# Kernel tuning notes

Measured on AMD Instinct MI355X. Metric: run time of the kernel, lower is better.

The kernel has to match this reference:

```python
import jax, jax.numpy as jnp
import numpy as np

S, M, E, K, C = 4096, 512, 16, 2, 128
H1, H2, H3 = 500, 500, 2000
SAMPLE = int(np.percentile(np.arange(S), 90))  # = 3685, matches int(np.percentile(idx_set, 90))
KMUL, KNUM = 2.0, 5


def setup_inputs() -> dict:
    key = jax.random.key(0)
    ks = jax.random.split(key, 8)
    def init(k, shape, fan):
        return (jax.random.normal(k, shape, jnp.float32) / np.float32(np.sqrt(fan)))
    inp = {
        'x': jax.random.normal(ks[0], (S, M), jnp.float32),
        'noise': jax.random.uniform(ks[1], (S, E), jnp.float32),
        'Wr': jnp.zeros((E, M), jnp.float32),  # router weight is zeroed in reset_parameters
        'W1': init(ks[2], (E, H1, M), M), 'b1': jnp.zeros((E, H1), jnp.float32),
        'W2': init(ks[3], (E, H2, H1), H1), 'b2': jnp.zeros((E, H2), jnp.float32),
        'W3': init(ks[4], (E, H3, H2), H2), 'b3': jnp.zeros((E, H3), jnp.float32),
        'W4': init(ks[5], (E, C, H3), H3), 'b4': jnp.zeros((E, C), jnp.float32),
    }
    rng = np.random.RandomState(0)
    npairs = K * (K - 1) // 2
    inp['idx1'] = jnp.asarray(np.stack([rng.choice(S, SAMPLE, replace=False) for _ in range(npairs)]).astype(np.int32))
    inp['idx2'] = jnp.asarray(np.stack([rng.choice(S, SAMPLE, replace=False) for _ in range(npairs)]).astype(np.int32))
    return inp


def _mmd(source, target):
    # Gaussian-kernel MMD, same math as MMD_loss (fix_sigma=None path).
    ns = source.shape[0]
    n = ns + target.shape[0]
    total = jnp.concatenate([source, target], axis=0)            # [n, d]
    sq = jnp.sum(total * total, axis=-1)
    d2 = sq[:, None] + sq[None, :] - 2.0 * (total @ total.T)     # [n, n] squared L2
    bw = jax.lax.stop_gradient(d2).sum() / (n * n - n)           # .data in torch => stop_gradient
    bw = bw / (KMUL ** (KNUM // 2))
    kern = jnp.zeros_like(d2)
    for i in range(KNUM):
        kern = kern + jnp.exp(-d2 / (bw * (KMUL ** i)))
    xx = kern[:ns, :ns]
    yy = kern[ns:, ns:]
    xy = kern[:ns, ns:]
    yx = kern[ns:, :ns]
    return jnp.mean(xx + yy - xy - yx)


def _forward(x, noise, Wr, W1, b1, W2, b2, W3, b3, W4, b4, idx1, idx2):
    select = x @ Wr.T + noise                                    # [S, E]
    gate, index = jax.lax.top_k(select, K)                       # [S, K]
    mask = jax.nn.one_hot(index, E, dtype=select.dtype)          # [S, K, E]
    density = mask.mean(axis=-2)                                 # [S, E]
    density_proxy = select.mean(axis=-2)                         # [E]
    balance_loss = jnp.mean(density_proxy * density) * float(E ** 2)
    mask_flat = mask.sum(axis=-1)                                # [S, K] (all ones)
    combine = jnp.transpose(gate[..., None] * mask_flat[..., None] * mask, (0, 2, 1))  # [S, E, K]
    dispatch = (combine != 0).astype(combine.dtype)              # bool().to(dtype)
    select0 = dispatch
    expert_inputs = jnp.einsum('sm,sec->ecm', x, dispatch)       # [E, K, M]
    h = jax.nn.relu(jnp.einsum('ecm,ehm->ech', expert_inputs, W1) + b1[:, None, :])
    h = jax.nn.relu(jnp.einsum('ech,egh->ecg', h, W2) + b2[:, None, :])
    h = jax.nn.relu(jnp.einsum('ecg,efg->ecf', h, W3) + b3[:, None, :])
    eout = jnp.einsum('ecf,edf->ecd', h, W4) + b4[:, None, :]    # [E, K, C]
    middle = jnp.transpose(jnp.einsum('sec,ecm->scm', combine, eout), (1, 0, 2))  # [K, S, C]
    output = jnp.einsum('sec,ecm->sm', combine, eout)            # [S, C]
    dist_loss = jnp.float32(0.0)
    p = 0
    for i in range(K):
        for j in range(i + 1, K):
            dist_loss = dist_loss - _mmd(middle[i][idx1[p]], middle[j][idx2[p]])
            p += 1
    return output, select0, balance_loss, dist_loss


def reference(x, noise, Wr, W1, b1, W2, b2, W3, b3, W4, b4, idx1, idx2):
    return _forward(x, noise, Wr, W1, b1, W2, b2, W3, b3, W4, b4, idx1, idx2)
```

## Files before the change

kernel.cpp:

```cpp
#include <hip/hip_runtime.h>

constexpr int S = 4096, M = 512, E = 16, CC = 128;
constexpr int H1 = 500, H2 = 500, H3 = 2000;
constexpr int TB = 256;

__global__ void k_route(const float* __restrict__ x, const float* __restrict__ noise,
                        const float* __restrict__ Wr, int* __restrict__ i0, int* __restrict__ i1,
                        float* __restrict__ g0, float* __restrict__ g1,
                        float* __restrict__ sel0, float* __restrict__ selpart,
                        int* __restrict__ counters) {
  if (blockIdx.x == 0 && threadIdx.x == 0) { counters[0] = 0; }
  int wid = threadIdx.x >> 6, lane = threadIdx.x & 63;
  int s = blockIdx.x * 4 + wid;
  const float* xr = x + (size_t)s * M;
  float xv[8];
#pragma unroll
  for (int c = 0; c < 8; ++c) xv[c] = xr[lane + 64 * c];
  float v[E];
#pragma unroll
  for (int e = 0; e < E; ++e) {
    const float* wr = Wr + (size_t)e * M;
    float acc = 0.f;
#pragma unroll
    for (int c = 0; c < 8; ++c) acc = fmaf(xv[c], wr[lane + 64 * c], acc);
#pragma unroll
    for (int off = 32; off; off >>= 1) acc += __shfl_xor(acc, off);
    v[e] = acc + noise[s * E + e];
  }
  int a0 = 0; float m0 = v[0];
#pragma unroll
  for (int e = 1; e < E; ++e) if (v[e] > m0) { m0 = v[e]; a0 = e; }
  int a1 = -1; float m1 = -3.4e38f;
#pragma unroll
  for (int e = 0; e < E; ++e) if (e != a0 && v[e] > m1) { m1 = v[e]; a1 = e; }
  __shared__ float vsh[4][16];
  if (lane < 16) vsh[wid][lane] = v[lane];
  if (lane == 0) { i0[s] = a0; i1[s] = a1; g0[s] = m0; g1[s] = m1; }
  if (lane < 16) {
    int e = lane;
    sel0[(size_t)s * 32 + e * 2 + 0] = (e == a0 && m0 != 0.f) ? 1.f : 0.f;
    sel0[(size_t)s * 32 + e * 2 + 1] = (e == a1 && m1 != 0.f) ? 1.f : 0.f;
  }
  __syncthreads();
  if (threadIdx.x < 16) {
    int e = threadIdx.x;
    selpart[blockIdx.x * 16 + e] = vsh[0][e] + vsh[1][e] + vsh[2][e] + vsh[3][e];
  }
}

__global__ __launch_bounds__(1024) void k_gather(const float* __restrict__ x,
                        const int* __restrict__ i0, const int* __restrict__ i1,
                        const float* __restrict__ g0, const float* __restrict__ g1,
                        float* __restrict__ ei) {
  __shared__ int rsi[S];
  __shared__ float rsg[S];
  __shared__ float gacc[8][128];
  int b = blockIdx.x;
  int chunk = b & 3, ek = b >> 2;
  int k = ek & 1, e = ek >> 1;
  const int* route = k ? i1 : i0;
  const float* gg = k ? g1 : g0;
  int t = threadIdx.x;
  for (int i = t; i < S; i += 1024) { rsi[i] = route[i]; rsg[i] = gg[i]; }
  __syncthreads();
  int g = t >> 7, dl = t & 127;
  int d = chunk * 128 + dl;
  float acc = 0.f;
  int q0 = g * 512;
  for (int q = q0; q < q0 + 512; ++q) {
    if (rsi[q] == e && rsg[q] != 0.f) acc += x[(size_t)q * M + d];
  }
  gacc[g][dl] = acc;
  __syncthreads();
  if (t < 128) {
    float ssum = 0.f;
#pragma unroll
    for (int g2 = 0; g2 < 8; ++g2) ssum += gacc[g2][t];
    ei[ek * M + chunk * 128 + t] = ssum;
  }
}

template <int DIN, int HOUT, bool RELU>
__global__ void k_layer(const float* __restrict__ in, const float* __restrict__ W,
                        const float* __restrict__ bias, float* __restrict__ out) {
  int w = (blockIdx.x * blockDim.x + threadIdx.x) >> 6;
  int lane = threadIdx.x & 63;
  if (w >= E * HOUT) return;
  int e = w / HOUT, h = w - e * HOUT;
  const float* wr = W + ((size_t)e * HOUT + h) * DIN;
  const float* in0 = in + (size_t)(e * 2 + 0) * DIN;
  const float* in1 = in + (size_t)(e * 2 + 1) * DIN;
  float a0 = 0.f, a1 = 0.f;
  for (int m = lane; m < DIN; m += 64) {
    float wv = wr[m];
    a0 += wv * in0[m];
    a1 += wv * in1[m];
  }
#pragma unroll
  for (int off = 32; off; off >>= 1) {
    a0 += __shfl_xor(a0, off);
    a1 += __shfl_xor(a1, off);
  }
  if (lane == 0) {
    float bb = bias[e * HOUT + h];
    float o0 = a0 + bb, o1 = a1 + bb;
    if (RELU) { o0 = fmaxf(o0, 0.f); o1 = fmaxf(o1, 0.f); }
    out[(size_t)(e * 2 + 0) * HOUT + h] = o0;
    out[(size_t)(e * 2 + 1) * HOUT + h] = o1;
  }
}

__global__ __launch_bounds__(256) void k_gprep(const float* __restrict__ eo,
                        const float* __restrict__ selpart,
                        const int* __restrict__ idx1, const int* __restrict__ idx2,
                        const int* __restrict__ i0, const int* __restrict__ i1,
                        const float* __restrict__ g0, const float* __restrict__ g1,
                        float* __restrict__ G32, float* __restrict__ rowg,
                        int* __restrict__ rowe, float* __restrict__ wpart,
                        int* __restrict__ cpart,
                        float* __restrict__ outb, int ns, int ncnt, int npad) {
  int t = threadIdx.x;
  if (blockIdx.x == 0) {
    __shared__ float Es[32 * 132];
    __shared__ double red_d[256];
    __shared__ float dpl[16];
    for (int i = t; i < 32 * 128; i += 256) Es[(i >> 7) * 132 + (i & 127)] = eo[i];
    __syncthreads();
    for (int p = t; p < 1024; p += 256) {
      int u = p >> 5, v = p & 31;
      float s = 0.f;
#pragma unroll 8
      for (int d = 0; d < 128; ++d) s = fmaf(Es[u * 132 + d], Es[v * 132 + d], s);
      G32[p] = s;
    }
    int e2 = t & 15, r0 = t >> 4;
    double acc = 0.0;
    for (int b2 = r0; b2 < 1024; b2 += 16) acc += (double)selpart[b2 * 16 + e2];
    red_d[t] = acc;
    __syncthreads();
    for (int off = 128; off >= 16; off >>= 1) { if (t < off) red_d[t] += red_d[t + off]; __syncthreads(); }
    if (t < 16) dpl[t] = (float)(red_d[t] / (double)S);
    __syncthreads();
    double acc2 = 0.0;
    for (int s2 = t; s2 < S; s2 += 256) acc2 += 0.5 * ((double)dpl[i0[s2]] + (double)dpl[i1[s2]]);
    red_d[t] = acc2;
    __syncthreads();
    for (int off = 128; off; off >>= 1) { if (t < off) red_d[t] += red_d[t + off]; __syncthreads(); }
    if (t == 0) outb[0] = (float)(red_d[0] / 256.0);
    return;
  }
  int blk = blockIdx.x - 1;
  int r = blk * 256 + t;
  float g = 0.f; int ek = 0;
  bool valid = (r < npad);
  if (r < ns)        { int tk = idx1[r];      ek = i0[tk] * 2 + 0; g = g0[tk]; }
  else if (r < ncnt) { int tk = idx2[r - ns]; ek = i1[tk] * 2 + 1; g = g1[tk]; }
  if (valid) { rowg[r] = g; rowe[r] = ek; }
  int ekb = valid ? ek : -1;
  __shared__ float sw[4][32], sw2[4][32];
  __shared__ int sc[4][32];
  int lane = t & 63, w = t >> 6;
  float g2 = g * g;
  for (int e = 0; e < 32; ++e) {
    unsigned long long m = __ballot(ekb == e);
    float vw = (ekb == e) ? g : 0.f;
    float vw2 = (ekb == e) ? g2 : 0.f;
#pragma unroll
    for (int off = 32; off; off >>= 1) { vw += __shfl_xor(vw, off); vw2 += __shfl_xor(vw2, off); }
    if (lane == 0) { sw[w][e] = vw; sw2[w][e] = vw2; sc[w][e] = __popcll(m); }
  }
  __syncthreads();
  if (t < 32) {
    wpart[blk * 64 + t]      = sw[0][t] + sw[1][t] + sw[2][t] + sw[3][t];
    wpart[blk * 64 + 32 + t] = sw2[0][t] + sw2[1][t] + sw2[2][t] + sw2[3][t];
    cpart[blk * 32 + t]      = sc[0][t] + sc[1][t] + sc[2][t] + sc[3][t];
  }
}

__global__ __launch_bounds__(256) void k_mid(const float* __restrict__ G32,
                        const float* __restrict__ wpart, const int* __restrict__ cpart,
                        const float* __restrict__ rowg, const int* __restrict__ rowe,
                        float* __restrict__ srowg, float* __restrict__ srowA,
                        int* __restrict__ srowe, float* __restrict__ srowsg,
                        float* __restrict__ cl2,
                        int ns, int ncnt, int npad, int nrowblk) {
  __shared__ int cpl[32 * 32];
  __shared__ int total_s[32];
  __shared__ int offmy[32];
  __shared__ float wf[32], w2f[32];
  __shared__ double redd[256];
  __shared__ int wcnt[4][32];
  __shared__ float c_sh;
  int t = threadIdx.x, blk = blockIdx.x;
  for (int i = t; i < nrowblk * 32; i += 256) cpl[i] = cpart[i];
  if (t < 32) {
    float sw = 0.f, sw2 = 0.f;
    for (int b = 0; b < nrowblk; ++b) { sw += wpart[b * 64 + t]; sw2 += wpart[b * 64 + 32 + t]; }
    wf[t] = sw; w2f[t] = sw2;
  }
  __syncthreads();
  if (t < 32) {
    int tot = 0;
    for (int b = 0; b < nrowblk; ++b) tot += cpl[b * 32 + t];
    total_s[t] = tot;
  }
  __syncthreads();
  if (t < 32) {
    int off = 0;
    for (int e = 0; e < t; ++e) off += total_s[e];
    for (int b = 0; b < blk; ++b) off += cpl[b * 32 + t];
    offmy[t] = off;
  }
  double part = 0.0;
  for (int i = t; i < 1024; i += 256)
    part += (double)wf[i >> 5] * (double)wf[i & 31] * (double)G32[i];
  redd[t] = part;
  __syncthreads();
  for (int off = 128; off; off >>= 1) { if (t < off) redd[t] += redd[t + off]; __syncthreads(); }
  double wGw = redd[0];
  __syncthreads();
  redd[t] = (t < 32) ? (double)w2f[t] * (double)G32[t * 33] : 0.0;
  __syncthreads();
  for (int off = 128; off; off >>= 1) { if (t < off) redd[t] += redd[t + off]; __syncthreads(); }
  if (t == 0) {
    double nn = (double)ncnt;
    double sumd2 = 2.0 * nn * redd[0] - 2.0 * wGw;
    double bw = sumd2 / (nn * nn - nn) / 4.0;
    c_sh = (float)(1.0 / (bw * 16.0));
    if (blk == 0) cl2[0] = c_sh;
  }
  __syncthreads();
  float c = c_sh;
  int r = blk * 256 + t;
  bool valid = (r < npad);
  float g = valid ? rowg[r] : 0.f;
  int ek = valid ? rowe[r] : -1;
  float sg = (r < ns) ? 1.f : (r < ncnt ? -1.f : 0.f);
  int lane = t & 63, w = t >> 6;
  int myrank = 0;
  for (int e = 0; e < 32; ++e) {
    unsigned long long m = __ballot(ek == e);
    if (ek == e) myrank = __popcll(m & ((1ull << lane) - 1ull));
    if (lane == 0) wcnt[w][e] = __popcll(m);
  }
  __syncthreads();
  if (valid) {
    int woff = 0;
    for (int w2 = 0; w2 < w; ++w2) woff += wcnt[w2][ek];
    int dest = offmy[ek] + woff + myrank;
    srowg[dest] = g;
    srowsg[dest] = sg;
    srowe[dest] = ek;
    srowA[dest] = c * g * g * G32[ek * 33];
  }
}

__global__ __launch_bounds__(512) void k_tail(const float* __restrict__ eo,
                      const int* __restrict__ i0, const int* __restrict__ i1,
                      const float* __restrict__ g0, const float* __restrict__ g1,
                      float* __restrict__ out,
                      const float* __restrict__ srowg, const float* __restrict__ srowA,
                      const int* __restrict__ srowe, const float* __restrict__ srowsg,
                      const float* __restrict__ G32, const float* __restrict__ cl2,
                      double* __restrict__ bsum, float* __restrict__ out_dist,
                      int ns, int ncnt, int nt, int ntri, int* __restrict__ counters) {
  int b = blockIdx.x, tid = threadIdx.x;
  if (b >= ntri) {
    int idx = (b - ntri) * 512 + tid;
    int s = idx >> 7, d = idx & (CC - 1);
    out[idx] = g0[s] * eo[(i0[s] * 2 + 0) * CC + d] + g1[s] * eo[(i1[s] * 2 + 1) * CC + d];
    return;
  }
  __shared__ float K2[1056];
  __shared__ float gAs[264], aAs[264], sAs[264];
  __shared__ int   eAs[264];
  __shared__ float gBs[264], aBs[264], sBs[264];
  __shared__ int   eBs[264];
  __shared__ float wred[8];
  __shared__ double redd[512];
  __shared__ int lastflag;

  int L = b;
  int bi = 0, rem = L;
  while (rem >= nt - bi) { rem -= nt - bi; ++bi; }
  int bj = bi + rem;
  const int ib = bi * TB, jb = bj * TB;

  float c = cl2[0];
  for (int i = tid; i < 1024; i += 512) K2[(i >> 5) * 33 + (i & 31)] = 2.f * c * G32[i];
  if (tid < TB) {
    int r = tid, p = (r & 7) * 33 + (r >> 3);
    gAs[p] = srowg[ib + r]; aAs[p] = srowA[ib + r];
    eAs[p] = srowe[ib + r] * 33; sAs[p] = srowsg[ib + r];
  } else {
    int r = tid - TB, p = (r & 7) * 33 + (r >> 3);
    gBs[p] = srowg[jb + r]; aBs[p] = srowA[jb + r];
    eBs[p] = srowe[jb + r]; sBs[p] = srowsg[jb + r];
  }
  __syncthreads();

  int ti = tid & 15, tjj = tid >> 4;
  float gj[8], Aj[8], sgj[8]; int ej[8];
#pragma unroll
  for (int q = 0; q < 8; ++q) {
    int p = q * 33 + tjj;
    gj[q] = gBs[p]; Aj[q] = aBs[p]; ej[q] = eBs[p]; sgj[q] = sBs[p];
  }
  float tsum = 0.f;
#pragma unroll
  for (int rb = 0; rb < 2; ++rb) {
    float gi[8], Ai[8], sgi[8]; int ei[8];
#pragma unroll
    for (int r = 0; r < 8; ++r) {
      int p = r * 33 + ti * 2 + rb;
      gi[r] = gAs[p]; Ai[r] = aAs[p]; ei[r] = eAs[p]; sgi[r] = sAs[p];
    }
#pragma unroll
    for (int r = 0; r < 8; ++r) {
#pragma unroll
      for (int q = 0; q < 8; ++q) {
        float gg = gi[r] * gj[q];
        float arg = fmaf(K2[ei[r] + ej[q]], gg, -(Ai[r] + Aj[q]));
        float t = __expf(arg);
        float t2 = t * t;   float s5 = t + t2;
        float t4 = t2 * t2; s5 += t4;
        float t8 = t4 * t4; s5 += t8;
        float t16 = t8 * t8; s5 += t16;
        tsum = fmaf(sgi[r] * sgj[q], s5, tsum);
      }
    }
  }
#pragma unroll
  for (int off = 32; off; off >>= 1) tsum += __shfl_xor(tsum, off);
  if ((tid & 63) == 0) wred[tid >> 6] = tsum;
  __syncthreads();
  if (tid == 0) {
    float sblk = 0.f;
#pragma unroll
    for (int w = 0; w < 8; ++w) sblk += wred[w];
    bsum[L] = (double)sblk * ((bi == bj) ? 1.0 : 2.0);
  }

  if (tid == 0) {
    __threadfence();
    int old = atomicAdd(&counters[0], 1);
    lastflag = (old == ntri - 1) ? 1 : 0;
  }
  __syncthreads();
  if (!lastflag) return;
  __threadfence();
  double acc = 0.0;
  for (int i = tid; i < ntri; i += 512) acc += bsum[i];
  redd[tid] = acc;
  __syncthreads();
  for (int off = 256; off; off >>= 1) { if (tid < off) redd[tid] += redd[tid + off]; __syncthreads(); }
  if (tid == 0) out_dist[0] = (float)(-redd[0] / ((double)ns * (double)ns));
}

extern "C" void kernel_launch(void* const* d_in, const int* in_sizes, int n_in,
                              void* d_out, int out_size, void* d_ws, size_t ws_size,
                              hipStream_t stream) {
  const float* x  = (const float*)d_in[0];
  const float* noise = (const float*)d_in[1];
  const float* Wr = (const float*)d_in[2];
  const float* W1 = (const float*)d_in[3];
  const float* b1 = (const float*)d_in[4];
  const float* W2 = (const float*)d_in[5];
  const float* b2 = (const float*)d_in[6];
  const float* W3 = (const float*)d_in[7];
  const float* b3 = (const float*)d_in[8];
  const float* W4 = (const float*)d_in[9];
  const float* b4 = (const float*)d_in[10];
  const int* idx1 = (const int*)d_in[11];
  const int* idx2 = (const int*)d_in[12];
  int ns = in_sizes[11];
  int n = 2 * ns;
  int npad = (n + 255) & ~255;
  int nt = npad / TB;
  int ntri = nt * (nt + 1) / 2;
  int nrowblk = npad / 256;

  char* wp = (char*)d_ws;
  size_t off = 0;
  auto alloc = [&](size_t bytes) -> void* {
    void* p = wp + off;
    off += (bytes + 255) & ~(size_t)255;
    return p;
  };
  int*   i0  = (int*)alloc((size_t)S * 4);
  int*   i1  = (int*)alloc((size_t)S * 4);
  float* g0  = (float*)alloc((size_t)S * 4);
  float* g1  = (float*)alloc((size_t)S * 4);
  float* selpart = (float*)alloc((size_t)1024 * 16 * 4);
  float* ei  = (float*)alloc((size_t)E * 2 * M * 4);
  float* h1  = (float*)alloc((size_t)E * 2 * H1 * 4);
  float* h2  = (float*)alloc((size_t)E * 2 * H2 * 4);
  float* h3  = (float*)alloc((size_t)E * 2 * H3 * 4);
  float* eo  = (float*)alloc((size_t)E * 2 * CC * 4);
  float* G32 = (float*)alloc((size_t)1024 * 4);
  float* rowg = (float*)alloc((size_t)npad * 4);
  int*   rowe = (int*)alloc((size_t)npad * 4);
  float* wpart = (float*)alloc((size_t)nrowblk * 64 * 4);
  int*   cpart = (int*)alloc((size_t)nrowblk * 32 * 4);
  float* srowg = (float*)alloc((size_t)npad * 4);
  float* srowA = (float*)alloc((size_t)npad * 4);
  int*   srowe = (int*)alloc((size_t)npad * 4);
  float* srowsg = (float*)alloc((size_t)npad * 4);
  float* cl2 = (float*)alloc(16);
  double* bsum = (double*)alloc((size_t)ntri * 8);
  int* counters = (int*)alloc(256);
  (void)ws_size; (void)n_in; (void)out_size;

  float* out      = (float*)d_out;
  float* out_sel0 = out + (size_t)S * CC;
  float* out_bal  = out + (size_t)S * CC + (size_t)S * E * 2;
  float* out_dist = out_bal + 1;

  k_route<<<S / 4, 256, 0, stream>>>(x, noise, Wr, i0, i1, g0, g1, out_sel0, selpart, counters);
  k_gather<<<128, 1024, 0, stream>>>(x, i0, i1, g0, g1, ei);
  k_layer<M, H1, true><<<(E * H1 + 3) / 4, 256, 0, stream>>>(ei, W1, b1, h1);
  k_layer<H1, H2, true><<<(E * H2 + 3) / 4, 256, 0, stream>>>(h1, W2, b2, h2);
  k_layer<H2, H3, true><<<(E * H3 + 3) / 4, 256, 0, stream>>>(h2, W3, b3, h3);
  k_layer<H3, CC, false><<<(E * CC + 3) / 4, 256, 0, stream>>>(h3, W4, b4, eo);
  k_gprep<<<1 + nrowblk, 256, 0, stream>>>(eo, selpart, idx1, idx2, i0, i1, g0, g1,
                                           G32, rowg, rowe, wpart, cpart, out_bal, ns, n, npad);
  k_mid<<<nrowblk, 256, 0, stream>>>(G32, wpart, cpart, rowg, rowe,
                                     srowg, srowA, srowe, srowsg, cl2, ns, n, npad, nrowblk);
  k_tail<<<ntri + (S * CC) / 512, 512, 0, stream>>>(eo, i0, i1, g0, g1, out, srowg, srowA,
                                                    srowe, srowsg, G32, cl2, bsum, out_dist,
                                                    ns, n, nt, ntri, counters);
}
```

Baseline: 158.5 us.

## Split expert gather across token segments with a separate reduction kernel

The gather that sums routed token rows per expert/slot is split from 128 large blocks into 1024 small blocks, each covering one 512-token segment and writing partial sums. A new kernel then reduces the eight segment partials into the expert input buffer. This is meant to spread the gather over more CUs and hide latency better. The cost is an extra kernel launch and a partial-sum buffer round trip through global memory.

```diff
diff --git a/kernel.cpp b/kernel.cpp
--- a/kernel.cpp
+++ b/kernel.cpp
@@ -48,36 +48,39 @@
   }
 }
 
-__global__ __launch_bounds__(1024) void k_gather(const float* __restrict__ x,
+__global__ __launch_bounds__(128) void k_gpart(const float* __restrict__ x,
                         const int* __restrict__ i0, const int* __restrict__ i1,
                         const float* __restrict__ g0, const float* __restrict__ g1,
-                        float* __restrict__ ei) {
-  __shared__ int rsi[S];
-  __shared__ float rsg[S];
-  __shared__ float gacc[8][128];
+                        float* __restrict__ gpart) {
+  __shared__ int rsi[512];
+  __shared__ float rsg[512];
   int b = blockIdx.x;
-  int chunk = b & 3, ek = b >> 2;
+  int seg = b & 7, chunk = (b >> 3) & 3, ek = b >> 5;
   int k = ek & 1, e = ek >> 1;
   const int* route = k ? i1 : i0;
   const float* gg = k ? g1 : g0;
   int t = threadIdx.x;
-  for (int i = t; i < S; i += 1024) { rsi[i] = route[i]; rsg[i] = gg[i]; }
-  __syncthreads();
-  int g = t >> 7, dl = t & 127;
-  int d = chunk * 128 + dl;
+  int s0 = seg * 512;
+#pragma unroll
+  for (int i = 0; i < 4; ++i) {
+    rsi[t + i * 128] = route[s0 + t + i * 128];
+    rsg[t + i * 128] = gg[s0 + t + i * 128];
+  }
+  __syncthreads();
+  int d = chunk * 128 + t;
   float acc = 0.f;
-  int q0 = g * 512;
-  for (int q = q0; q < q0 + 512; ++q) {
-    if (rsi[q] == e && rsg[q] != 0.f) acc += x[(size_t)q * M + d];
-  }
-  gacc[g][dl] = acc;
-  __syncthreads();
-  if (t < 128) {
-    float ssum = 0.f;
-#pragma unroll
-    for (int g2 = 0; g2 < 8; ++g2) ssum += gacc[g2][t];
-    ei[ek * M + chunk * 128 + t] = ssum;
-  }
+  for (int q = 0; q < 512; ++q) {
+    if (rsi[q] == e && rsg[q] != 0.f) acc += x[(size_t)(s0 + q) * M + d];
+  }
+  gpart[(size_t)seg * (32 * M) + ek * M + d] = acc;
+}
+
+__global__ void k_gred(const float* __restrict__ gpart, float* __restrict__ ei) {
+  int idx = blockIdx.x * blockDim.x + threadIdx.x;
+  float acc = 0.f;
+#pragma unroll
+  for (int sg = 0; sg < 8; ++sg) acc += gpart[(size_t)sg * (32 * M) + idx];
+  ei[idx] = acc;
 }
 
 template <int DIN, int HOUT, bool RELU>
@@ -392,6 +395,7 @@
   float* g0  = (float*)alloc((size_t)S * 4);
   float* g1  = (float*)alloc((size_t)S * 4);
   float* selpart = (float*)alloc((size_t)1024 * 16 * 4);
+  float* gpart = (float*)alloc((size_t)8 * 32 * M * 4);
   float* ei  = (float*)alloc((size_t)E * 2 * M * 4);
   float* h1  = (float*)alloc((size_t)E * 2 * H1 * 4);
   float* h2  = (float*)alloc((size_t)E * 2 * H2 * 4);
@@ -417,7 +421,8 @@
   float* out_dist = out_bal + 1;
 
   k_route<<<S / 4, 256, 0, stream>>>(x, noise, Wr, i0, i1, g0, g1, out_sel0, selpart, counters);
-  k_gather<<<128, 1024, 0, stream>>>(x, i0, i1, g0, g1, ei);
+  k_gpart<<<1024, 128, 0, stream>>>(x, i0, i1, g0, g1, gpart);
+  k_gred<<<64, 256, 0, stream>>>(gpart, ei);
   k_layer<M, H1, true><<<(E * H1 + 3) / 4, 256, 0, stream>>>(ei, W1, b1, h1);
   k_layer<H1, H2, true><<<(E * H2 + 3) / 4, 256, 0, stream>>>(h1, W2, b2, h2);
   k_layer<H2, H3, true><<<(E * H3 + 3) / 4, 256, 0, stream>>>(h2, W3, b3, h3);
```

Result: faster. 155.0 us (-2.2%).
